# Performance work log

Hardware: AMD Instinct MI355X
Metric: run time of the kernel (lower is better)

Reference implementation:

```python
import jax, jax.numpy as jnp
import numpy as np

N_NODES = 100000
N_EDGES = 640000
IN_DIM, HID_DIM, OUT_DIM = 128, 64, 32


def setup_inputs() -> dict:
    key = jax.random.key(0)
    ks = jax.random.split(key, 8)
    x = jax.random.normal(ks[0], (N_NODES, IN_DIM), dtype=jnp.float32)
    edge_index = jax.random.randint(ks[1], (2, N_EDGES), 0, N_NODES, dtype=jnp.int64)
    # SAGEConv params: lin_l (applied to aggregated neighbors, has bias),
    # lin_r (applied to root node, no bias) -- PyG defaults.
    s1 = 1.0 / np.sqrt(IN_DIM)
    s2 = 1.0 / np.sqrt(HID_DIM)
    W1l = jax.random.uniform(ks[2], (HID_DIM, IN_DIM), jnp.float32, -s1, s1)
    b1 = jax.random.uniform(ks[3], (HID_DIM,), jnp.float32, -s1, s1)
    W1r = jax.random.uniform(ks[4], (HID_DIM, IN_DIM), jnp.float32, -s1, s1)
    W2l = jax.random.uniform(ks[5], (OUT_DIM, HID_DIM), jnp.float32, -s2, s2)
    b2 = jax.random.uniform(ks[6], (OUT_DIM,), jnp.float32, -s2, s2)
    W2r = jax.random.uniform(ks[7], (OUT_DIM, HID_DIM), jnp.float32, -s2, s2)
    return {"x": x, "edge_index": edge_index,
            "W1l": W1l, "b1": b1, "W1r": W1r,
            "W2l": W2l, "b2": b2, "W2r": W2r}


def _sage_conv(x, src, dst, Wl, b, Wr, num_nodes):
    # mean aggregation of source features onto destination nodes
    msg = x[src]                                                # [E, d]
    agg = jax.ops.segment_sum(msg, dst, num_segments=num_nodes)  # [N, d]
    cnt = jax.ops.segment_sum(jnp.ones((src.shape[0],), x.dtype), dst,
                              num_segments=num_nodes)            # [N]
    agg = agg / jnp.maximum(cnt, 1.0)[:, None]
    # out = lin_l(mean_neighbors) + lin_r(x)
    return agg @ Wl.T + b + x @ Wr.T


def reference(x, edge_index, W1l, b1, W1r, W2l, b2, W2r):
    src, dst = edge_index[0], edge_index[1]
    n = x.shape[0]
    h = jax.nn.relu(_sage_conv(x, src, dst, W1l, b1, W1r, n))
    out = _sage_conv(h, src, dst, W2l, b2, W2r, n)
    return out
```

## Files before the change

kernel.cpp:

```cpp
#include <hip/hip_runtime.h>
#include <hip/hip_bf16.h>

typedef __hip_bfloat16 bf16;
typedef __attribute__((ext_vector_type(8))) short short8;
typedef __attribute__((ext_vector_type(4))) float f32x4;

#define N_NODES 100000
#define N_EDGES 640000
#define NSB 98
#define N_TILES 6250
#define GE 313
#define HB 625
#define LIN1_BLKS 1024

__device__ __forceinline__ float bf2f(short s) {
    union { float f; unsigned u; } u;
    u.u = ((unsigned)(unsigned short)s) << 16;
    return u.f;
}
__device__ __forceinline__ short f2s(float f) {
    union { bf16 b; short s; } u;
    u.b = __float2bfloat16(f);
    return u.s;
}

__device__ __forceinline__ int detect_is64(const int* __restrict__ idx) {
    int lane = threadIdx.x & 63;
    int v = idx[2 * (lane & 31) + 1];
    return __ballot(v == 0) == ~0ULL;
}
__device__ __forceinline__ int detect_f32(const unsigned* __restrict__ xw) {
    int lane = threadIdx.x & 63;
    unsigned e = (xw[lane] >> 7) & 0xFFu;
    int inr = (e >= 0x20u && e <= 0x4Fu);
    return __popcll(__ballot(inr)) < 48;
}

__device__ __forceinline__ void decode8(
        const int* __restrict__ eidx, int is64, int e0, int E,
        int (&ss)[8], int (&dd)[8]) {
    if (is64) {
        int4 a0 = *(const int4*)&eidx[2 * e0];
        int4 a1 = *(const int4*)&eidx[2 * e0 + 4];
        int4 a2 = *(const int4*)&eidx[2 * e0 + 8];
        int4 a3 = *(const int4*)&eidx[2 * e0 + 12];
        int4 b0 = *(const int4*)&eidx[2 * (E + e0)];
        int4 b1 = *(const int4*)&eidx[2 * (E + e0) + 4];
        int4 b2 = *(const int4*)&eidx[2 * (E + e0) + 8];
        int4 b3 = *(const int4*)&eidx[2 * (E + e0) + 12];
        ss[0] = a0.x; ss[1] = a0.z; ss[2] = a1.x; ss[3] = a1.z;
        ss[4] = a2.x; ss[5] = a2.z; ss[6] = a3.x; ss[7] = a3.z;
        dd[0] = b0.x; dd[1] = b0.z; dd[2] = b1.x; dd[3] = b1.z;
        dd[4] = b2.x; dd[5] = b2.z; dd[6] = b3.x; dd[7] = b3.z;
    } else {
        int4 s0 = *(const int4*)&eidx[e0];
        int4 s1 = *(const int4*)&eidx[e0 + 4];
        int4 d0 = *(const int4*)&eidx[E + e0];
        int4 d1 = *(const int4*)&eidx[E + e0 + 4];
        ss[0] = s0.x; ss[1] = s0.y; ss[2] = s0.z; ss[3] = s0.w;
        ss[4] = s1.x; ss[5] = s1.y; ss[6] = s1.z; ss[7] = s1.w;
        dd[0] = d0.x; dd[1] = d0.y; dd[2] = d0.z; dd[3] = d0.w;
        dd[4] = d1.x; dd[5] = d1.y; dd[6] = d1.z; dd[7] = d1.w;
    }
}

__device__ __forceinline__ void decode4(
        const int* __restrict__ eidx, int is64, int e0, int E,
        int (&ss)[4], int (&dd)[4]) {
    if (is64) {
        int4 a0 = *(const int4*)&eidx[2 * e0];
        int4 a1 = *(const int4*)&eidx[2 * e0 + 4];
        int4 b0 = *(const int4*)&eidx[2 * (E + e0)];
        int4 b1 = *(const int4*)&eidx[2 * (E + e0) + 4];
        ss[0] = a0.x; ss[1] = a0.z; ss[2] = a1.x; ss[3] = a1.z;
        dd[0] = b0.x; dd[1] = b0.z; dd[2] = b1.x; dd[3] = b1.z;
    } else {
        int4 s0 = *(const int4*)&eidx[e0];
        int4 d0 = *(const int4*)&eidx[E + e0];
        ss[0] = s0.x; ss[1] = s0.y; ss[2] = s0.z; ss[3] = s0.w;
        dd[0] = d0.x; dd[1] = d0.y; dd[2] = d0.z; dd[3] = d0.w;
    }
}

__global__ __launch_bounds__(256) void hist_kernel(
        const int* __restrict__ eidx, int* __restrict__ deg,
        int* __restrict__ rank) {
    const int is64 = detect_is64(eidx);
    const int e0 = (blockIdx.x * 256 + threadIdx.x) * 4;
    int ss[4], dd[4], rk[4];
    decode4(eidx, is64, e0, N_EDGES, ss, dd);
#pragma unroll
    for (int c = 0; c < 4; ++c) {
        bool ok = (unsigned)ss[c] < (unsigned)N_NODES &&
                  (unsigned)dd[c] < (unsigned)N_NODES;
        rk[c] = ok ? atomicAdd(&deg[dd[c]], 1) : 0;
    }
    *(int4*)&rank[e0] = make_int4(rk[0], rk[1], rk[2], rk[3]);
}

__device__ __forceinline__ short8 load_frag(const void* base, size_t eoff, int f32) {
    if (f32) {
        const float4* p = (const float4*)((const float*)base + eoff);
        const float4 u = p[0], v = p[1];
        short8 r;
        r[0] = f2s(u.x); r[1] = f2s(u.y); r[2] = f2s(u.z); r[3] = f2s(u.w);
        r[4] = f2s(v.x); r[5] = f2s(v.y); r[6] = f2s(v.z); r[7] = f2s(v.w);
        return r;
    }
    return *(const short8*)((const short*)base + eoff);
}

__global__ __launch_bounds__(256) void lin1_kernel(
        const void* __restrict__ x, const void* __restrict__ W1l,
        const void* __restrict__ W1r, bf16* __restrict__ xl,
        bf16* __restrict__ xr) {
    const int f32 = detect_f32((const unsigned*)x);
    __shared__ short wlds[2][16][64][8];

    const int tid = threadIdx.x;
    {
        const int l = tid & 63, fg = tid >> 6;
        const int mm = l & 15, qq = l >> 4;
#pragma unroll
        for (int i = 0; i < 4; ++i) {
            const int f = fg * 4 + i;
            const int ks = f >> 2, dt = f & 3;
            const size_t wo = (size_t)(dt * 16 + mm) * 128 + ks * 32 + qq * 8;
            *(short8*)&wlds[0][f][l][0] = load_frag(W1l, wo, f32);
            *(short8*)&wlds[1][f][l][0] = load_frag(W1r, wo, f32);
        }
    }
    __syncthreads();

    const int nwaves = LIN1_BLKS * 4;
    const int wid = blockIdx.x * 4 + (tid >> 6);
    const int lane = tid & 63;
    const int m = lane & 15, quad = lane >> 4;
    const short* wl0 = &wlds[0][0][lane][0];
    const short* wr0 = &wlds[1][0][lane][0];

    int tile = wid;
    if (tile >= N_TILES) return;

    short8 a[4];
    {
        const size_t arow = (size_t)(tile * 16 + m) * 128 + quad * 8;
#pragma unroll
        for (int ks = 0; ks < 4; ++ks)
            a[ks] = load_frag(x, arow + ks * 32, f32);
    }

    while (true) {
        const int nxt = tile + nwaves;
        short8 an[4];
        if (nxt < N_TILES) {
            const size_t arow = (size_t)(nxt * 16 + m) * 128 + quad * 8;
#pragma unroll
            for (int ks = 0; ks < 4; ++ks)
                an[ks] = load_frag(x, arow + ks * 32, f32);
        }

        f32x4 accl[4], accr[4];
#pragma unroll
        for (int dt = 0; dt < 4; ++dt) {
            accl[dt] = (f32x4){0.f, 0.f, 0.f, 0.f};
            accr[dt] = (f32x4){0.f, 0.f, 0.f, 0.f};
        }
#pragma unroll
        for (int ks = 0; ks < 4; ++ks)
#pragma unroll
            for (int dt = 0; dt < 4; ++dt) {
                const short8 wl = *(const short8*)(wl0 + (ks * 4 + dt) * 512);
                const short8 wr = *(const short8*)(wr0 + (ks * 4 + dt) * 512);
                accl[dt] = __builtin_amdgcn_mfma_f32_16x16x32_bf16(
                    wl, a[ks], accl[dt], 0, 0, 0);
                accr[dt] = __builtin_amdgcn_mfma_f32_16x16x32_bf16(
                    wr, a[ks], accr[dt], 0, 0, 0);
            }

        const int node = tile * 16 + m;
#pragma unroll
        for (int dt = 0; dt < 4; ++dt) {
            short4 pl, pr;
            pl.x = f2s(accl[dt][0]); pl.y = f2s(accl[dt][1]);
            pl.z = f2s(accl[dt][2]); pl.w = f2s(accl[dt][3]);
            pr.x = f2s(accr[dt][0]); pr.y = f2s(accr[dt][1]);
            pr.z = f2s(accr[dt][2]); pr.w = f2s(accr[dt][3]);
            *(short4*)((short*)xl + (size_t)node * 64 + dt * 16 + quad * 4) = pl;
            *(short4*)((short*)xr + (size_t)node * 64 + dt * 16 + quad * 4) = pr;
        }

        if (nxt >= N_TILES) break;
        tile = nxt;
#pragma unroll
        for (int ks = 0; ks < 4; ++ks) a[ks] = an[ks];
    }
}

__global__ __launch_bounds__(256) void scan_partial_kernel(
        const int* __restrict__ deg, int* __restrict__ off,
        int* __restrict__ bsum, int N) {
    __shared__ int ss[256];
    const int tid = threadIdx.x, blk = blockIdx.x;
    const int base = blk * 1024 + tid * 4;
    int v[4], s = 0;
    if (base + 3 < N) {
        int4 dv = *(const int4*)&deg[base];
        v[0] = dv.x; v[1] = dv.y; v[2] = dv.z; v[3] = dv.w;
    } else {
#pragma unroll
        for (int c = 0; c < 4; ++c) v[c] = (base + c < N) ? deg[base + c] : 0;
    }
#pragma unroll
    for (int c = 0; c < 4; ++c) s += v[c];
    ss[tid] = s; __syncthreads();
    for (int o = 1; o < 256; o <<= 1) {
        int t = (tid >= o) ? ss[tid - o] : 0;
        __syncthreads();
        ss[tid] += t;
        __syncthreads();
    }
    int run = ss[tid] - s;
    if (tid == 255) bsum[blk] = ss[255];
#pragma unroll
    for (int c = 0; c < 4; ++c) {
        if (base + c < N) off[base + c] = run;
        run += v[c];
    }
}

__global__ __launch_bounds__(256) void scan_add_kernel(
        int* __restrict__ off, const int* __restrict__ bsum, int N) {
    __shared__ int ss[NSB];
    const int blk = blockIdx.x, tid = threadIdx.x;
    if (tid < NSB) ss[tid] = bsum[tid];
    __syncthreads();
    int add = 0;
    for (int i = 0; i < blk; ++i) add += ss[i];
    const int base = blk * 1024 + tid * 4;
#pragma unroll
    for (int c = 0; c < 4; ++c) {
        int i = base + c;
        if (i < N) off[i] += add;
    }
    if (blk == NSB - 1 && tid == 0)
        off[N] = add + ss[NSB - 1];
}

__global__ __launch_bounds__(256) void fill_kernel(
        const int* __restrict__ eidx, const int* __restrict__ off,
        const int* __restrict__ rank, int* __restrict__ srcs, int E, int N) {
    const int is64 = detect_is64(eidx);
    int e0 = (blockIdx.x * 256 + threadIdx.x) * 8;
    if (e0 >= E) return;
    int ss[8], dd[8];
    decode8(eidx, is64, e0, E, ss, dd);
    int4 r0 = *(const int4*)&rank[e0];
    int4 r1 = *(const int4*)&rank[e0 + 4];
    const int rk[8] = {r0.x, r0.y, r0.z, r0.w, r1.x, r1.y, r1.z, r1.w};
#pragma unroll
    for (int c = 0; c < 8; ++c) {
        if ((unsigned)ss[c] >= (unsigned)N || (unsigned)dd[c] >= (unsigned)N) continue;
        srcs[off[dd[c]] + rk[c]] = ss[c];
    }
}

__global__ __launch_bounds__(256) void gather1_lin2_kernel(
        const int* __restrict__ srcs, const int* __restrict__ off,
        const bf16* __restrict__ xl, const bf16* __restrict__ xr,
        const void* __restrict__ b1, const void* __restrict__ W2l,
        const void* __restrict__ W2r, bf16* __restrict__ hl,
        bf16* __restrict__ hr, const unsigned* __restrict__ xdet) {
    const int f32 = detect_f32(xdet);
    const int tid = threadIdx.x;
    const int lane = tid & 63, wave = tid >> 6;
    const int m = lane & 15, quad = lane >> 4;

    const void* Wb = (wave < 2) ? W2l : W2r;
    short8 bfrag[2];
#pragma unroll
    for (int ks = 0; ks < 2; ++ks)
        bfrag[ks] = load_frag(
            Wb, (size_t)((wave & 1) * 16 + m) * 64 + ks * 32 + quad * 8, f32);

    __shared__ short htile[16][72];

    const int node = blockIdx.x * 16 + (tid >> 4);
    const int j = tid & 15;
    const int gbase = lane & ~15;
    const int a = off[node], b = off[node + 1];
    float a0 = 0.f, a1 = 0.f, a2 = 0.f, a3 = 0.f;
    for (int base = a; base < b; base += 16) {
        const int cdeg = min(b - base, 16);
        int sv = (j < cdeg) ? srcs[base + j] : 0;
        for (int bb = 0; bb < cdeg; bb += 8) {
            short4 v[8];
#pragma unroll
            for (int t = 0; t < 8; ++t) {
                const int idx = bb + t;
                const int s = __shfl(sv, gbase + (idx < cdeg ? idx : 0));
                if (idx < cdeg)
                    v[t] = *(const short4*)((const short*)xl + (size_t)s * 64 + j * 4);
                else
                    v[t] = make_short4(0, 0, 0, 0);
            }
#pragma unroll
            for (int t = 0; t < 8; ++t) {
                a0 += bf2f(v[t].x); a1 += bf2f(v[t].y);
                a2 += bf2f(v[t].z); a3 += bf2f(v[t].w);
            }
        }
    }
    float b0, b1v, b2v, b3;
    if (f32) {
        float4 bb4 = *(const float4*)((const float*)b1 + j * 4);
        b0 = bb4.x; b1v = bb4.y; b2v = bb4.z; b3 = bb4.w;
    } else {
        short4 bb4 = *(const short4*)((const short*)b1 + j * 4);
        b0 = bf2f(bb4.x); b1v = bf2f(bb4.y); b2v = bf2f(bb4.z); b3 = bf2f(bb4.w);
    }
    short4 xr4 = *(const short4*)((const short*)xr + (size_t)node * 64 + j * 4);
    const float inv = 1.0f / fmaxf((float)(b - a), 1.0f);
    short4 o;
    o.x = f2s(fmaxf(a0 * inv + b0  + bf2f(xr4.x), 0.0f));
    o.y = f2s(fmaxf(a1 * inv + b1v + bf2f(xr4.y), 0.0f));
    o.z = f2s(fmaxf(a2 * inv + b2v + bf2f(xr4.z), 0.0f));
    o.w = f2s(fmaxf(a3 * inv + b3  + bf2f(xr4.w), 0.0f));
    *(short4*)&htile[tid >> 4][j * 4] = o;
    __syncthreads();

    short8 afr[2];
#pragma unroll
    for (int ks = 0; ks < 2; ++ks)
        afr[ks] = *(const short8*)&htile[m][ks * 32 + quad * 8];
    f32x4 acc = (f32x4){0.f, 0.f, 0.f, 0.f};
#pragma unroll
    for (int ks = 0; ks < 2; ++ks)
        acc = __builtin_amdgcn_mfma_f32_16x16x32_bf16(
            bfrag[ks], afr[ks], acc, 0, 0, 0);

    bf16* dst = (wave < 2) ? hl : hr;
    const int onode = blockIdx.x * 16 + m;
    short4 p;
    p.x = f2s(acc[0]); p.y = f2s(acc[1]);
    p.z = f2s(acc[2]); p.w = f2s(acc[3]);
    *(short4*)((short*)dst + (size_t)onode * 32 + (wave & 1) * 16 + quad * 4) = p;
}

__global__ __launch_bounds__(256) void gather2_kernel(
        const int* __restrict__ srcs, const int* __restrict__ off,
        const bf16* __restrict__ hl, const bf16* __restrict__ hr,
        const void* __restrict__ b2, void* __restrict__ out,
        const unsigned* __restrict__ xdet, int N) {
    const int f32 = detect_f32(xdet);
    const int tid = threadIdx.x;
    const int node = blockIdx.x * 32 + (tid >> 3);
    const int j = tid & 7;
    const int gbase = (tid & 63) & ~7;
    const int a = off[node], b = off[node + 1];
    float a0 = 0.f, a1 = 0.f, a2 = 0.f, a3 = 0.f;
    for (int base = a; base < b; base += 8) {
        const int cdeg = min(b - base, 8);
        int sv = (j < cdeg) ? srcs[base + j] : 0;
        short4 v[8];
#pragma unroll
        for (int t = 0; t < 8; ++t) {
            const int s = __shfl(sv, gbase + (t < cdeg ? t : 0));
            if (t < cdeg)
                v[t] = *(const short4*)((const short*)hl + (size_t)s * 32 + j * 4);
            else
                v[t] = make_short4(0, 0, 0, 0);
        }
#pragma unroll
        for (int t = 0; t < 8; ++t) {
            a0 += bf2f(v[t].x); a1 += bf2f(v[t].y);
            a2 += bf2f(v[t].z); a3 += bf2f(v[t].w);
        }
    }
    float b0, b1v, b2v, b3;
    if (f32) {
        float4 bb4 = *(const float4*)((const float*)b2 + j * 4);
        b0 = bb4.x; b1v = bb4.y; b2v = bb4.z; b3 = bb4.w;
    } else {
        short4 bb4 = *(const short4*)((const short*)b2 + j * 4);
        b0 = bf2f(bb4.x); b1v = bf2f(bb4.y); b2v = bf2f(bb4.z); b3 = bf2f(bb4.w);
    }
    short4 hr4 = *(const short4*)((const short*)hr + (size_t)node * 32 + j * 4);
    const float inv = 1.0f / fmaxf((float)(b - a), 1.0f);
    const float v0 = a0 * inv + b0  + bf2f(hr4.x);
    const float v1 = a1 * inv + b1v + bf2f(hr4.y);
    const float v2 = a2 * inv + b2v + bf2f(hr4.z);
    const float v3 = a3 * inv + b3  + bf2f(hr4.w);
    if (f32) {
        *(float4*)((float*)out + (size_t)node * 32 + j * 4) =
            make_float4(v0, v1, v2, v3);
    } else {
        short4 o;
        o.x = f2s(v0); o.y = f2s(v1); o.z = f2s(v2); o.w = f2s(v3);
        *(short4*)((short*)out + (size_t)node * 32 + j * 4) = o;
    }
}

extern "C" void kernel_launch(void* const* d_in, const int* in_sizes, int n_in,
                              void* d_out, int out_size, void* d_ws, size_t ws_size,
                              hipStream_t stream) {
    const void* x   = d_in[0];
    const int*  eix = (const int*)d_in[1];
    const void* W1l = d_in[2];
    const void* b1  = d_in[3];
    const void* W1r = d_in[4];
    const void* W2l = d_in[5];
    const void* b2  = d_in[6];
    const void* W2r = d_in[7];

    const int N = N_NODES;
    const int E = N_EDGES;

    char* ws = (char*)d_ws;
    bf16*  xl    = (bf16*)(ws + 256);
    bf16*  xr    = (bf16*)(ws + 256 + (size_t)N * 128);
    bf16*  hl    = (bf16*)(ws + 256 + (size_t)N * 384);
    bf16*  hr    = (bf16*)(ws + 256 + (size_t)N * 448);
    int*   off   = (int*) (ws + 256 + (size_t)N * 512);
    int*   deg   = off + (N + 4);
    int*   rank  = deg + N;
    int*   srcs  = rank + E;
    int*   bsum  = srcs + E;

    hipMemsetAsync(deg, 0, (size_t)N * 4, stream);

    hist_kernel<<<HB, 256, 0, stream>>>(eix, deg, rank);

    scan_partial_kernel<<<NSB, 256, 0, stream>>>(deg, off, bsum, N);
    scan_add_kernel<<<NSB, 256, 0, stream>>>(off, bsum, N);
    fill_kernel<<<GE, 256, 0, stream>>>(eix, off, rank, srcs, E, N);

    lin1_kernel<<<LIN1_BLKS, 256, 0, stream>>>(x, W1l, W1r, xl, xr);

    gather1_lin2_kernel<<<N / 16, 256, 0, stream>>>(
        srcs, off, xl, xr, b1, W2l, W2r, hl, hr, (const unsigned*)x);

    gather2_kernel<<<N / 32, 256, 0, stream>>>(
        srcs, off, hl, hr, b2, d_out, (const unsigned*)x, N);
}
```

Before: 208.0 us.

## Drop rank buffer via decrementing atomics in fill; widen gather loads to 16B

The histogram kernel no longer records a per-edge rank. Instead, the fill kernel computes each slot position by atomically decrementing the degree counter, which removes the rank write and read traffic. Both gather kernels now have each lane load 8 bf16 values (16 bytes) per neighbour instead of 4, so fewer lanes serve each node. gather1 now handles 32 nodes per block and issues two MFMA node tiles. The cost is more atomics in fill, a nondeterministic neighbour order within each CSR row, and possibly lower parallelism per node in the gathers.

Result: slower. 220.4 us (+6.0%).

```diff
diff --git a/kernel.cpp b/kernel.cpp
--- a/kernel.cpp
+++ b/kernel.cpp
@@ -9,9 +9,10 @@
 #define N_EDGES 640000
 #define NSB 98
 #define N_TILES 6250
-#define GE 313
-#define HB 625
+#define EB 625
 #define LIN1_BLKS 1024
+#define G1_BLKS 3125
+#define G2_BLKS 1563
 
 __device__ __forceinline__ float bf2f(short s) {
     union { float f; unsigned u; } u;
@@ -34,34 +35,6 @@
     unsigned e = (xw[lane] >> 7) & 0xFFu;
     int inr = (e >= 0x20u && e <= 0x4Fu);
     return __popcll(__ballot(inr)) < 48;
-}
-
-__device__ __forceinline__ void decode8(
-        const int* __restrict__ eidx, int is64, int e0, int E,
-        int (&ss)[8], int (&dd)[8]) {
-    if (is64) {
-        int4 a0 = *(const int4*)&eidx[2 * e0];
-        int4 a1 = *(const int4*)&eidx[2 * e0 + 4];
-        int4 a2 = *(const int4*)&eidx[2 * e0 + 8];
-        int4 a3 = *(const int4*)&eidx[2 * e0 + 12];
-        int4 b0 = *(const int4*)&eidx[2 * (E + e0)];
-        int4 b1 = *(const int4*)&eidx[2 * (E + e0) + 4];
-        int4 b2 = *(const int4*)&eidx[2 * (E + e0) + 8];
-        int4 b3 = *(const int4*)&eidx[2 * (E + e0) + 12];
-        ss[0] = a0.x; ss[1] = a0.z; ss[2] = a1.x; ss[3] = a1.z;
-        ss[4] = a2.x; ss[5] = a2.z; ss[6] = a3.x; ss[7] = a3.z;
-        dd[0] = b0.x; dd[1] = b0.z; dd[2] = b1.x; dd[3] = b1.z;
-        dd[4] = b2.x; dd[5] = b2.z; dd[6] = b3.x; dd[7] = b3.z;
-    } else {
-        int4 s0 = *(const int4*)&eidx[e0];
-        int4 s1 = *(const int4*)&eidx[e0 + 4];
-        int4 d0 = *(const int4*)&eidx[E + e0];
-        int4 d1 = *(const int4*)&eidx[E + e0 + 4];
-        ss[0] = s0.x; ss[1] = s0.y; ss[2] = s0.z; ss[3] = s0.w;
-        ss[4] = s1.x; ss[5] = s1.y; ss[6] = s1.z; ss[7] = s1.w;
-        dd[0] = d0.x; dd[1] = d0.y; dd[2] = d0.z; dd[3] = d0.w;
-        dd[4] = d1.x; dd[5] = d1.y; dd[6] = d1.z; dd[7] = d1.w;
-    }
 }
 
 __device__ __forceinline__ void decode4(
@@ -83,117 +56,16 @@
 }
 
 __global__ __launch_bounds__(256) void hist_kernel(
-        const int* __restrict__ eidx, int* __restrict__ deg,
-        int* __restrict__ rank) {
+        const int* __restrict__ eidx, int* __restrict__ deg) {
     const int is64 = detect_is64(eidx);
     const int e0 = (blockIdx.x * 256 + threadIdx.x) * 4;
-    int ss[4], dd[4], rk[4];
+    int ss[4], dd[4];
     decode4(eidx, is64, e0, N_EDGES, ss, dd);
 #pragma unroll
     for (int c = 0; c < 4; ++c) {
-        bool ok = (unsigned)ss[c] < (unsigned)N_NODES &&
-                  (unsigned)dd[c] < (unsigned)N_NODES;
-        rk[c] = ok ? atomicAdd(&deg[dd[c]], 1) : 0;
-    }
-    *(int4*)&rank[e0] = make_int4(rk[0], rk[1], rk[2], rk[3]);
-}
-
-__device__ __forceinline__ short8 load_frag(const void* base, size_t eoff, int f32) {
-    if (f32) {
-        const float4* p = (const float4*)((const float*)base + eoff);
-        const float4 u = p[0], v = p[1];
-        short8 r;
-        r[0] = f2s(u.x); r[1] = f2s(u.y); r[2] = f2s(u.z); r[3] = f2s(u.w);
-        r[4] = f2s(v.x); r[5] = f2s(v.y); r[6] = f2s(v.z); r[7] = f2s(v.w);
-        return r;
-    }
-    return *(const short8*)((const short*)base + eoff);
-}
-
-__global__ __launch_bounds__(256) void lin1_kernel(
-        const void* __restrict__ x, const void* __restrict__ W1l,
-        const void* __restrict__ W1r, bf16* __restrict__ xl,
-        bf16* __restrict__ xr) {
-    const int f32 = detect_f32((const unsigned*)x);
-    __shared__ short wlds[2][16][64][8];
-
-    const int tid = threadIdx.x;
-    {
-        const int l = tid & 63, fg = tid >> 6;
-        const int mm = l & 15, qq = l >> 4;
-#pragma unroll
-        for (int i = 0; i < 4; ++i) {
-            const int f = fg * 4 + i;
-            const int ks = f >> 2, dt = f & 3;
-            const size_t wo = (size_t)(dt * 16 + mm) * 128 + ks * 32 + qq * 8;
-            *(short8*)&wlds[0][f][l][0] = load_frag(W1l, wo, f32);
-            *(short8*)&wlds[1][f][l][0] = load_frag(W1r, wo, f32);
-        }
-    }
-    __syncthreads();
-
-    const int nwaves = LIN1_BLKS * 4;
-    const int wid = blockIdx.x * 4 + (tid >> 6);
-    const int lane = tid & 63;
-    const int m = lane & 15, quad = lane >> 4;
-    const short* wl0 = &wlds[0][0][lane][0];
-    const short* wr0 = &wlds[1][0][lane][0];
-
-    int tile = wid;
-    if (tile >= N_TILES) return;
-
-    short8 a[4];
-    {
-        const size_t arow = (size_t)(tile * 16 + m) * 128 + quad * 8;
-#pragma unroll
-        for (int ks = 0; ks < 4; ++ks)
-            a[ks] = load_frag(x, arow + ks * 32, f32);
-    }
-
-    while (true) {
-        const int nxt = tile + nwaves;
-        short8 an[4];
-        if (nxt < N_TILES) {
-            const size_t arow = (size_t)(nxt * 16 + m) * 128 + quad * 8;
-#pragma unroll
-            for (int ks = 0; ks < 4; ++ks)
-                an[ks] = load_frag(x, arow + ks * 32, f32);
-        }
-
-        f32x4 accl[4], accr[4];
-#pragma unroll
-        for (int dt = 0; dt < 4; ++dt) {
-            accl[dt] = (f32x4){0.f, 0.f, 0.f, 0.f};
-            accr[dt] = (f32x4){0.f, 0.f, 0.f, 0.f};
-        }
-#pragma unroll
-        for (int ks = 0; ks < 4; ++ks)
-#pragma unroll
-            for (int dt = 0; dt < 4; ++dt) {
-                const short8 wl = *(const short8*)(wl0 + (ks * 4 + dt) * 512);
-                const short8 wr = *(const short8*)(wr0 + (ks * 4 + dt) * 512);
-                accl[dt] = __builtin_amdgcn_mfma_f32_16x16x32_bf16(
-                    wl, a[ks], accl[dt], 0, 0, 0);
-                accr[dt] = __builtin_amdgcn_mfma_f32_16x16x32_bf16(
-                    wr, a[ks], accr[dt], 0, 0, 0);
-            }
-
-        const int node = tile * 16 + m;
-#pragma unroll
-        for (int dt = 0; dt < 4; ++dt) {
-            short4 pl, pr;
-            pl.x = f2s(accl[dt][0]); pl.y = f2s(accl[dt][1]);
-            pl.z = f2s(accl[dt][2]); pl.w = f2s(accl[dt][3]);
-            pr.x = f2s(accr[dt][0]); pr.y = f2s(accr[dt][1]);
-            pr.z = f2s(accr[dt][2]); pr.w = f2s(accr[dt][3]);
-            *(short4*)((short*)xl + (size_t)node * 64 + dt * 16 + quad * 4) = pl;
-            *(short4*)((short*)xr + (size_t)node * 64 + dt * 16 + quad * 4) = pr;
-        }
-
-        if (nxt >= N_TILES) break;
-        tile = nxt;
-#pragma unroll
-        for (int ks = 0; ks < 4; ++ks) a[ks] = an[ks];
+        if ((unsigned)ss[c] < (unsigned)N_NODES &&
+            (unsigned)dd[c] < (unsigned)N_NODES)
+            atomicAdd(&deg[dd[c]], 1);
     }
 }
 
@@ -249,19 +121,116 @@
 
 __global__ __launch_bounds__(256) void fill_kernel(
         const int* __restrict__ eidx, const int* __restrict__ off,
-        const int* __restrict__ rank, int* __restrict__ srcs, int E, int N) {
+        int* __restrict__ deg, int* __restrict__ srcs) {
     const int is64 = detect_is64(eidx);
-    int e0 = (blockIdx.x * 256 + threadIdx.x) * 8;
-    if (e0 >= E) return;
-    int ss[8], dd[8];
-    decode8(eidx, is64, e0, E, ss, dd);
-    int4 r0 = *(const int4*)&rank[e0];
-    int4 r1 = *(const int4*)&rank[e0 + 4];
-    const int rk[8] = {r0.x, r0.y, r0.z, r0.w, r1.x, r1.y, r1.z, r1.w};
-#pragma unroll
-    for (int c = 0; c < 8; ++c) {
-        if ((unsigned)ss[c] >= (unsigned)N || (unsigned)dd[c] >= (unsigned)N) continue;
-        srcs[off[dd[c]] + rk[c]] = ss[c];
+    const int e0 = (blockIdx.x * 256 + threadIdx.x) * 4;
+    int ss[4], dd[4];
+    decode4(eidx, is64, e0, N_EDGES, ss, dd);
+#pragma unroll
+    for (int c = 0; c < 4; ++c) {
+        if ((unsigned)ss[c] >= (unsigned)N_NODES ||
+            (unsigned)dd[c] >= (unsigned)N_NODES) continue;
+        const int pos = atomicAdd(&deg[dd[c]], -1) - 1;
+        srcs[off[dd[c]] + pos] = ss[c];
+    }
+}
+
+__device__ __forceinline__ short8 load_frag(const void* base, size_t eoff, int f32) {
+    if (f32) {
+        const float4* p = (const float4*)((const float*)base + eoff);
+        const float4 u = p[0], v = p[1];
+        short8 r;
+        r[0] = f2s(u.x); r[1] = f2s(u.y); r[2] = f2s(u.z); r[3] = f2s(u.w);
+        r[4] = f2s(v.x); r[5] = f2s(v.y); r[6] = f2s(v.z); r[7] = f2s(v.w);
+        return r;
+    }
+    return *(const short8*)((const short*)base + eoff);
+}
+
+__global__ __launch_bounds__(256) void lin1_kernel(
+        const void* __restrict__ x, const void* __restrict__ W1l,
+        const void* __restrict__ W1r, bf16* __restrict__ xl,
+        bf16* __restrict__ xr) {
+    const int f32 = detect_f32((const unsigned*)x);
+    __shared__ short wlds[2][16][64][8];
+
+    const int tid = threadIdx.x;
+    {
+        const int l = tid & 63, fg = tid >> 6;
+        const int mm = l & 15, qq = l >> 4;
+#pragma unroll
+        for (int i = 0; i < 4; ++i) {
+            const int f = fg * 4 + i;
+            const int ks = f >> 2, dt = f & 3;
+            const size_t wo = (size_t)(dt * 16 + mm) * 128 + ks * 32 + qq * 8;
+            *(short8*)&wlds[0][f][l][0] = load_frag(W1l, wo, f32);
+            *(short8*)&wlds[1][f][l][0] = load_frag(W1r, wo, f32);
+        }
+    }
+    __syncthreads();
+
+    const int nwaves = LIN1_BLKS * 4;
+    const int wid = blockIdx.x * 4 + (tid >> 6);
+    const int lane = tid & 63;
+    const int m = lane & 15, quad = lane >> 4;
+    const short* wl0 = &wlds[0][0][lane][0];
+    const short* wr0 = &wlds[1][0][lane][0];
+
+    int tile = wid;
+    if (tile >= N_TILES) return;
+
+    short8 a[4];
+    {
+        const size_t arow = (size_t)(tile * 16 + m) * 128 + quad * 8;
+#pragma unroll
+        for (int ks = 0; ks < 4; ++ks)
+            a[ks] = load_frag(x, arow + ks * 32, f32);
+    }
+
+    while (true) {
+        const int nxt = tile + nwaves;
+        short8 an[4];
+        if (nxt < N_TILES) {
+            const size_t arow = (size_t)(nxt * 16 + m) * 128 + quad * 8;
+#pragma unroll
+            for (int ks = 0; ks < 4; ++ks)
+                an[ks] = load_frag(x, arow + ks * 32, f32);
+        }
+
+        f32x4 accl[4], accr[4];
+#pragma unroll
+        for (int dt = 0; dt < 4; ++dt) {
+            accl[dt] = (f32x4){0.f, 0.f, 0.f, 0.f};
+            accr[dt] = (f32x4){0.f, 0.f, 0.f, 0.f};
+        }
+#pragma unroll
+        for (int ks = 0; ks < 4; ++ks)
+#pragma unroll
+            for (int dt = 0; dt < 4; ++dt) {
+                const short8 wl = *(const short8*)(wl0 + (ks * 4 + dt) * 512);
+                const short8 wr = *(const short8*)(wr0 + (ks * 4 + dt) * 512);
+                accl[dt] = __builtin_amdgcn_mfma_f32_16x16x32_bf16(
+                    wl, a[ks], accl[dt], 0, 0, 0);
+                accr[dt] = __builtin_amdgcn_mfma_f32_16x16x32_bf16(
+                    wr, a[ks], accr[dt], 0, 0, 0);
+            }
+
+        const int node = tile * 16 + m;
+#pragma unroll
+        for (int dt = 0; dt < 4; ++dt) {
+            short4 pl, pr;
+            pl.x = f2s(accl[dt][0]); pl.y = f2s(accl[dt][1]);
+            pl.z = f2s(accl[dt][2]); pl.w = f2s(accl[dt][3]);
+            pr.x = f2s(accr[dt][0]); pr.y = f2s(accr[dt][1]);
+            pr.z = f2s(accr[dt][2]); pr.w = f2s(accr[dt][3]);
+            *(short4*)((short*)xl + (size_t)node * 64 + dt * 16 + quad * 4) = pl;
+            *(short4*)((short*)xr + (size_t)node * 64 + dt * 16 + quad * 4) = pr;
+        }
+
+        if (nxt >= N_TILES) break;
+        tile = nxt;
+#pragma unroll
+        for (int ks = 0; ks < 4; ++ks) a[ks] = an[ks];
     }
 }
 
@@ -283,68 +252,70 @@
         bfrag[ks] = load_frag(
             Wb, (size_t)((wave & 1) * 16 + m) * 64 + ks * 32 + quad * 8, f32);
 
-    __shared__ short htile[16][72];
-
-    const int node = blockIdx.x * 16 + (tid >> 4);
-    const int j = tid & 15;
-    const int gbase = lane & ~15;
+    __shared__ short htile[32][72];
+
+    const int node = blockIdx.x * 32 + (tid >> 3);
+    const int j = tid & 7;
+    const int gbase = lane & ~7;
     const int a = off[node], b = off[node + 1];
-    float a0 = 0.f, a1 = 0.f, a2 = 0.f, a3 = 0.f;
-    for (int base = a; base < b; base += 16) {
-        const int cdeg = min(b - base, 16);
+    float acc[8] = {0.f, 0.f, 0.f, 0.f, 0.f, 0.f, 0.f, 0.f};
+    for (int base = a; base < b; base += 8) {
+        const int cdeg = min(b - base, 8);
         int sv = (j < cdeg) ? srcs[base + j] : 0;
-        for (int bb = 0; bb < cdeg; bb += 8) {
-            short4 v[8];
-#pragma unroll
-            for (int t = 0; t < 8; ++t) {
-                const int idx = bb + t;
-                const int s = __shfl(sv, gbase + (idx < cdeg ? idx : 0));
-                if (idx < cdeg)
-                    v[t] = *(const short4*)((const short*)xl + (size_t)s * 64 + j * 4);
-                else
-                    v[t] = make_short4(0, 0, 0, 0);
-            }
-#pragma unroll
-            for (int t = 0; t < 8; ++t) {
-                a0 += bf2f(v[t].x); a1 += bf2f(v[t].y);
-                a2 += bf2f(v[t].z); a3 += bf2f(v[t].w);
-            }
-        }
-    }
-    float b0, b1v, b2v, b3;
+        short8 v[8];
+#pragma unroll
+        for (int t = 0; t < 8; ++t) {
+            const int s = __shfl(sv, gbase + (t < cdeg ? t : 0));
+            if (t < cdeg)
+                v[t] = *(const short8*)((const short*)xl + (size_t)s * 64 + j * 8);
+            else
+                v[t] = (short8){0, 0, 0, 0, 0, 0, 0, 0};
+        }
+#pragma unroll
+        for (int t = 0; t < 8; ++t)
+#pragma unroll
+            for (int d = 0; d < 8; ++d) acc[d] += bf2f(v[t][d]);
+    }
+    float bias[8];
     if (f32) {
-        float4 bb4 = *(const float4*)((const float*)b1 + j * 4);
-        b0 = bb4.x; b1v = bb4.y; b2v = bb4.z; b3 = bb4.w;
+        float4 u = *(const float4*)((const float*)b1 + j * 8);
+        float4 w = *(const float4*)((const float*)b1 + j * 8 + 4);
+        bias[0] = u.x; bias[1] = u.y; bias[2] = u.z; bias[3] = u.w;
+        bias[4] = w.x; bias[5] = w.y; bias[6] = w.z; bias[7] = w.w;
     } else {
-        short4 bb4 = *(const short4*)((const short*)b1 + j * 4);
-        b0 = bf2f(bb4.x); b1v = bf2f(bb4.y); b2v = bf2f(bb4.z); b3 = bf2f(bb4.w);
-    }
-    short4 xr4 = *(const short4*)((const short*)xr + (size_t)node * 64 + j * 4);
+        short8 bb = *(const short8*)((const short*)b1 + j * 8);
+#pragma unroll
+        for (int d = 0; d < 8; ++d) bias[d] = bf2f(bb[d]);
+    }
+    short8 xr8 = *(const short8*)((const short*)xr + (size_t)node * 64 + j * 8);
     const float inv = 1.0f / fmaxf((float)(b - a), 1.0f);
-    short4 o;
-    o.x = f2s(fmaxf(a0 * inv + b0  + bf2f(xr4.x), 0.0f));
-    o.y = f2s(fmaxf(a1 * inv + b1v + bf2f(xr4.y), 0.0f));
-    o.z = f2s(fmaxf(a2 * inv + b2v + bf2f(xr4.z), 0.0f));
-    o.w = f2s(fmaxf(a3 * inv + b3  + bf2f(xr4.w), 0.0f));
-    *(short4*)&htile[tid >> 4][j * 4] = o;
+    short8 o;
+#pragma unroll
+    for (int d = 0; d < 8; ++d)
+        o[d] = f2s(fmaxf(acc[d] * inv + bias[d] + bf2f(xr8[d]), 0.0f));
+    *(short8*)&htile[tid >> 3][j * 8] = o;
     __syncthreads();
 
-    short8 afr[2];
-#pragma unroll
-    for (int ks = 0; ks < 2; ++ks)
-        afr[ks] = *(const short8*)&htile[m][ks * 32 + quad * 8];
-    f32x4 acc = (f32x4){0.f, 0.f, 0.f, 0.f};
-#pragma unroll
-    for (int ks = 0; ks < 2; ++ks)
-        acc = __builtin_amdgcn_mfma_f32_16x16x32_bf16(
-            bfrag[ks], afr[ks], acc, 0, 0, 0);
-
+    f32x4 acc2[2];
+#pragma unroll
+    for (int nt = 0; nt < 2; ++nt) {
+        acc2[nt] = (f32x4){0.f, 0.f, 0.f, 0.f};
+#pragma unroll
+        for (int ks = 0; ks < 2; ++ks) {
+            const short8 afr = *(const short8*)&htile[nt * 16 + m][ks * 32 + quad * 8];
+            acc2[nt] = __builtin_amdgcn_mfma_f32_16x16x32_bf16(
+                bfrag[ks], afr, acc2[nt], 0, 0, 0);
+        }
+    }
     bf16* dst = (wave < 2) ? hl : hr;
-    const int onode = blockIdx.x * 16 + m;
-    short4 p;
-    p.x = f2s(acc[0]); p.y = f2s(acc[1]);
-    p.z = f2s(acc[2]); p.w = f2s(acc[3]);
-    *(short4*)((short*)dst + (size_t)onode * 32 + (wave & 1) * 16 + quad * 4) = p;
+#pragma unroll
+    for (int nt = 0; nt < 2; ++nt) {
+        const int onode = blockIdx.x * 32 + nt * 16 + m;
+        short4 p;
+        p.x = f2s(acc2[nt][0]); p.y = f2s(acc2[nt][1]);
+        p.z = f2s(acc2[nt][2]); p.w = f2s(acc2[nt][3]);
+        *(short4*)((short*)dst + (size_t)onode * 32 + (wave & 1) * 16 + quad * 4) = p;
+    }
 }
 
 __global__ __launch_bounds__(256) void gather2_kernel(
@@ -354,50 +325,57 @@
         const unsigned* __restrict__ xdet, int N) {
     const int f32 = detect_f32(xdet);
     const int tid = threadIdx.x;
-    const int node = blockIdx.x * 32 + (tid >> 3);
-    const int j = tid & 7;
-    const int gbase = (tid & 63) & ~7;
-    const int a = off[node], b = off[node + 1];
-    float a0 = 0.f, a1 = 0.f, a2 = 0.f, a3 = 0.f;
-    for (int base = a; base < b; base += 8) {
-        const int cdeg = min(b - base, 8);
+    const int node = blockIdx.x * 64 + (tid >> 2);
+    const int j = tid & 3;
+    const int gbase = (tid & 63) & ~3;
+    const int valid = node < N;
+    int a = 0, b = 0;
+    if (valid) { a = off[node]; b = off[node + 1]; }
+    float acc[8] = {0.f, 0.f, 0.f, 0.f, 0.f, 0.f, 0.f, 0.f};
+    for (int base = a; base < b; base += 4) {
+        const int cdeg = min(b - base, 4);
         int sv = (j < cdeg) ? srcs[base + j] : 0;
-        short4 v[8];
-#pragma unroll
-        for (int t = 0; t < 8; ++t) {
+        short8 v[4];
+#pragma unroll
+        for (int t = 0; t < 4; ++t) {
             const int s = __shfl(sv, gbase + (t < cdeg ? t : 0));
             if (t < cdeg)
-                v[t] = *(const short4*)((const short*)hl + (size_t)s * 32 + j * 4);
+                v[t] = *(const short8*)((const short*)hl + (size_t)s * 32 + j * 8);
             else
-                v[t] = make_short4(0, 0, 0, 0);
-        }
-#pragma unroll
-        for (int t = 0; t < 8; ++t) {
-            a0 += bf2f(v[t].x); a1 += bf2f(v[t].y);
-            a2 += bf2f(v[t].z); a3 += bf2f(v[t].w);
-        }
-    }
-    float b0, b1v, b2v, b3;
+                v[t] = (short8){0, 0, 0, 0, 0, 0, 0, 0};
+        }
+#pragma unroll
+        for (int t = 0; t < 4; ++t)
+#pragma unroll
+            for (int d = 0; d < 8; ++d) acc[d] += bf2f(v[t][d]);
+    }
+    if (!valid) return;
+    float bias[8];
     if (f32) {
-        float4 bb4 = *(const float4*)((const float*)b2 + j * 4);
-        b0 = bb4.x; b1v = bb4.y; b2v = bb4.z; b3 = bb4.w;
+        float4 u = *(const float4*)((const float*)b2 + j * 8);
+        float4 w = *(const float4*)((const float*)b2 + j * 8 + 4);
+        bias[0] = u.x; bias[1] = u.y; bias[2] = u.z; bias[3] = u.w;
+        bias[4] = w.x; bias[5] = w.y; bias[6] = w.z; bias[7] = w.w;
     } else {
-        short4 bb4 = *(const short4*)((const short*)b2 + j * 4);
-        b0 = bf2f(bb4.x); b1v = bf2f(bb4.y); b2v = bf2f(bb4.z); b3 = bf2f(bb4.w);
-    }
-    short4 hr4 = *(const short4*)((const short*)hr + (size_t)node * 32 + j * 4);
+        short8 bb = *(const short8*)((const short*)b2 + j * 8);
+#pragma unroll
+        for (int d = 0; d < 8; ++d) bias[d] = bf2f(bb[d]);
+    }
+    short8 hr8 = *(const short8*)((const short*)hr + (size_t)node * 32 + j * 8);
     const float inv = 1.0f / fmaxf((float)(b - a), 1.0f);
-    const float v0 = a0 * inv + b0  + bf2f(hr4.x);
-    const float v1 = a1 * inv + b1v + bf2f(hr4.y);
-    const float v2 = a2 * inv + b2v + bf2f(hr4.z);
-    const float v3 = a3 * inv + b3  + bf2f(hr4.w);
+    float v[8];
+#pragma unroll
+    for (int d = 0; d < 8; ++d) v[d] = acc[d] * inv + bias[d] + bf2f(hr8[d]);
     if (f32) {
-        *(float4*)((float*)out + (size_t)node * 32 + j * 4) =
-            make_float4(v0, v1, v2, v3);
+        *(float4*)((float*)out + (size_t)node * 32 + j * 8) =
+            make_float4(v[0], v[1], v[2], v[3]);
+        *(float4*)((float*)out + (size_t)node * 32 + j * 8 + 4) =
+            make_float4(v[4], v[5], v[6], v[7]);
     } else {
-        short4 o;
-        o.x = f2s(v0); o.y = f2s(v1); o.z = f2s(v2); o.w = f2s(v3);
-        *(short4*)((short*)out + (size_t)node * 32 + j * 4) = o;
+        short8 o;
+#pragma unroll
+        for (int d = 0; d < 8; ++d) o[d] = f2s(v[d]);
+        *(short8*)((short*)out + (size_t)node * 32 + j * 8) = o;
     }
 }
 
@@ -414,7 +392,6 @@
     const void* W2r = d_in[7];
 
     const int N = N_NODES;
-    const int E = N_EDGES;
 
     char* ws = (char*)d_ws;
     bf16*  xl    = (bf16*)(ws + 256);
@@ -423,23 +400,23 @@
     bf16*  hr    = (bf16*)(ws + 256 + (size_t)N * 448);
     int*   off   = (int*) (ws + 256 + (size_t)N * 512);
     int*   deg   = off + (N + 4);
-    int*   rank  = deg + N;
-    int*   srcs  = rank + E;
-    int*   bsum  = srcs + E;
+    int*   srcs  = deg + N;
+    int*   bsum  = srcs + N_EDGES;
 
     hipMemsetAsync(deg, 0, (size_t)N * 4, stream);
 
-    hist_kernel<<<HB, 256, 0, stream>>>(eix, deg, rank);
+    hist_kernel<<<EB, 256, 0, stream>>>(eix, deg);
 
     scan_partial_kernel<<<NSB, 256, 0, stream>>>(deg, off, bsum, N);
     scan_add_kernel<<<NSB, 256, 0, stream>>>(off, bsum, N);
-    fill_kernel<<<GE, 256, 0, stream>>>(eix, off, rank, srcs, E, N);
+
+    fill_kernel<<<EB, 256, 0, stream>>>(eix, off, deg, srcs);
 
     lin1_kernel<<<LIN1_BLKS, 256, 0, stream>>>(x, W1l, W1r, xl, xr);
 
-    gather1_lin2_kernel<<<N / 16, 256, 0, stream>>>(
+    gather1_lin2_kernel<<<G1_BLKS, 256, 0, stream>>>(
         srcs, off, xl, xr, b1, W2l, W2r, hl, hr, (const unsigned*)x);
 
-    gather2_kernel<<<N / 32, 256, 0, stream>>>(
+    gather2_kernel<<<G2_BLKS, 256, 0, stream>>>(
         srcs, off, hl, hr, b2, d_out, (const unsigned*)x, N);
 }
```
